# Performance work log

Measured on AMD Instinct MI355X. Metric: run time of the kernel, lower is better.

## Reference

```python
import jax, jax.numpy as jnp
import numpy as np


def setup_inputs() -> dict:
    key = jax.random.key(0)
    ks = jax.random.split(key, 10)
    B, T = 1024, 8192
    # X features: [time, current I, temperature T, voltage U]
    t = jnp.cumsum(jax.random.uniform(ks[0], (B, T, 1), jnp.float32) + 0.5, axis=1)  # increasing time
    feats = jax.random.normal(ks[1], (B, T, 3), jnp.float32)
    X = jnp.concatenate([t, feats], axis=-1)  # [B, T, 4]
    # SC: [Q (capacity), eta_0, R, SOC_init_base]; keep Q away from 0
    SC = jax.random.uniform(ks[2], (B, 4), jnp.float32, minval=0.5, maxval=1.5)
    std = 0.1
    # SOC_init_net: Linear(4,1) -> Softplus -> Linear(1,1), normal(0,0.1) weights, zero bias
    W1i = jax.random.normal(ks[3], (1, 4), jnp.float32) * std
    b1i = jnp.zeros((1,), jnp.float32)
    W2i = jax.random.normal(ks[4], (1, 1), jnp.float32) * std
    b2i = jnp.zeros((1,), jnp.float32)
    # eta_net: Linear(2,1) -> Softplus -> Linear(1,1)
    W1e = jax.random.normal(ks[5], (1, 2), jnp.float32) * std
    b1e = jnp.zeros((1,), jnp.float32)
    W2e = jax.random.normal(ks[6], (1, 1), jnp.float32) * std
    b2e = jnp.zeros((1,), jnp.float32)
    return {"X": X, "SC": SC, "W1i": W1i, "b1i": b1i, "W2i": W2i, "b2i": b2i,
            "W1e": W1e, "b1e": b1e, "W2e": W2e, "b2e": b2e}


def reference(X, SC, W1i, b1i, W2i, b2i, W1e, b1e, W2e, b2e):
    # X: [B, T, 4] = (t, I, Temp, U); SC: [B, 4] = (Q, eta_0, R, soc_base)
    I = X[..., 1:2]      # [B, T, 1]
    Temp = X[..., 2:3]   # [B, T, 1]
    U = X[..., 3:4]      # [B, T, 1]
    R = SC[..., 2:3]     # [B, 1]
    # SOC_init_net on first-timestep features
    feat0 = jnp.concatenate([I[:, 0, :], Temp[:, 0, :], U[:, 0, :], R], axis=-1)  # [B, 4]
    h0 = jax.nn.softplus(feat0 @ W1i.T + b1i)
    soc_net = h0 @ W2i.T + b2i                     # [B, 1]
    SOC_init = SC[..., 3:4] * (1.0 + soc_net)      # [B, 1]
    # eta_net over all timesteps
    feat = jnp.concatenate([I, Temp], axis=-1)     # [B, T, 2]
    h = jax.nn.softplus(feat @ W1e.T + b1e)
    delta_eta = h @ W2e.T + b2e                    # [B, T, 1]
    # ODE RHS: dSOC/dt = eta_0 * (1 + delta_eta) * I / (3600 * Q)
    Q = SC[..., 0:1][:, None, :]                   # [B, 1, 1]
    eta0 = SC[..., 1:2][:, None, :]                # [B, 1, 1]
    f = eta0 * (1.0 + delta_eta) * I / (3600.0 * Q)  # [B, T, 1]
    # Euler integration: y_{k+1} = y_k + (t_{k+1} - t_k) * f(x_k, y_k); f independent of y -> cumsum
    ts = X[..., 0:1]                               # [B, T, 1]
    dt = ts[:, 1:] - ts[:, :-1]                    # [B, T-1, 1]
    incr = dt * f[:, :-1]                          # [B, T-1, 1]
    zero = jnp.zeros_like(SOC_init)[:, None, :]    # [B, 1, 1]
    SOC = SOC_init[:, None, :] + jnp.concatenate([zero, jnp.cumsum(incr, axis=1)], axis=1)
    return SOC                                     # [B, T, 1]
```

## Files before the change

### kernel.cpp

```cpp
#include <hip/hip_runtime.h>
#include <type_traits>


static __device__ __forceinline__ float bf2f(unsigned int u) {
    union { unsigned int i; float f; } v;
    v.i = u << 16;
    return v.f;
}
static __device__ __forceinline__ unsigned short f2bf(float f) {
    union { unsigned int i; float f; } v;
    v.f = f;
    unsigned int x = v.i;
    return (unsigned short)((x + 0x7fffu + ((x >> 16) & 1u)) >> 16);
}
static __device__ __forceinline__ float sp_fast(float x) {
    return __logf(1.f + __expf(x));
}

struct F4 { float ts, I, Te, U; };
static __device__ __forceinline__ F4 dec(ushort4 x) {
    return {bf2f(x.x), bf2f(x.y), bf2f(x.z), bf2f(x.w)};
}
static __device__ __forceinline__ F4 dec(float4 x) {
    return {x.x, x.y, x.z, x.w};
}

template <bool BF16>
static __device__ __forceinline__ float ld(const void* p, int i) {
    return BF16 ? bf2f(((const unsigned short*)p)[i]) : ((const float*)p)[i];
}

constexpr int BLOCK = 256;

template <bool BF16, int NC>
static __device__ void scan_reg(
    const void* __restrict__ Xv, const void* __restrict__ SCv,
    const void* __restrict__ W1i, const void* __restrict__ b1i,
    const void* __restrict__ W2i, const void* __restrict__ b2i,
    const void* __restrict__ W1e, const void* __restrict__ b1e,
    const void* __restrict__ W2e, const void* __restrict__ b2e,
    void* __restrict__ outv, float* s_wtot, float* s_init)
{
    using XVec = typename std::conditional<BF16, ushort4, float4>::type;
    constexpr int T = NC * 256;
    constexpr int SPAN = T / 4;

    const int b    = blockIdx.x;
    const int tid  = threadIdx.x;
    const int lane = tid & 63;
    const int wave = tid >> 6;
    const int wavestart = wave * SPAN;

    const float Q    = ld<BF16>(SCv, b * 4 + 0);
    const float eta0 = ld<BF16>(SCv, b * 4 + 1);
    const float R    = ld<BF16>(SCv, b * 4 + 2);
    const float S3   = ld<BF16>(SCv, b * 4 + 3);
    const float w1e0 = ld<BF16>(W1e, 0);
    const float w1e1 = ld<BF16>(W1e, 1);
    const float vb1e = ld<BF16>(b1e, 0);
    const float coef = eta0 / (3600.f * Q);
    const float c2   = coef * ld<BF16>(W2e, 0);
    const float c1   = coef * (1.f + ld<BF16>(b2e, 0));

    const XVec* Xrow = (const XVec*)Xv + (size_t)b * T;

    float ts_c, f_c;
    if (wave > 0) {
        const F4 vp = dec(Xrow[wavestart - 1]);
        const float hp = sp_fast(fmaf(vp.I, w1e0, fmaf(vp.Te, w1e1, vb1e)));
        f_c  = fmaf(c2, hp, c1) * vp.I;
        ts_c = vp.ts;
    } else {
        const F4 v0 = dec(Xrow[0]);
        ts_c = v0.ts;
        f_c  = 0.f;
        const float pre = fmaf(v0.I, ld<BF16>(W1i, 0),
                          fmaf(v0.Te, ld<BF16>(W1i, 1),
                          fmaf(v0.U, ld<BF16>(W1i, 2),
                          fmaf(R, ld<BF16>(W1i, 3), ld<BF16>(b1i, 0)))));
        const float h0 = sp_fast(pre);
        if (lane == 0)
            *s_init = S3 * (1.f + fmaf(h0, ld<BF16>(W2i, 0), ld<BF16>(b2i, 0)));
    }

    float vals[NC];
    float carry = 0.f;
    XVec cur = Xrow[wavestart + lane];
    XVec nxt = Xrow[wavestart + 64 + lane];
    #pragma unroll
    for (int c = 0; c < NC; ++c) {
        XVec after = cur;
        if (c + 2 < NC) after = Xrow[wavestart + (c + 2) * 64 + lane];

        const F4 v = dec(cur);
        const float f = fmaf(c2, sp_fast(fmaf(v.I, w1e0, fmaf(v.Te, w1e1, vb1e))), c1) * v.I;

        float pts = __shfl_up(v.ts, 1, 64);
        float pf  = __shfl_up(f,   1, 64);
        if (lane == 0) { pts = ts_c; pf = f_c; }
        float g = (v.ts - pts) * pf;

        #pragma unroll
        for (int d = 1; d < 64; d <<= 1) {
            const float u = __shfl_up(g, d, 64);
            if (lane >= d) g += u;
        }
        g += carry;
        vals[c] = g;

        carry = __shfl(g, 63, 64);
        ts_c  = __shfl(v.ts, 63, 64);
        f_c   = __shfl(f, 63, 64);
        cur = nxt; nxt = after;
    }
    if (lane == 0) s_wtot[wave] = carry;
    __syncthreads();

    float base = *s_init;
    #pragma unroll
    for (int w = 0; w < 3; ++w)
        if (w < wave) base += s_wtot[w];

    if (!BF16) {
        float* op = (float*)outv + (size_t)b * T + wavestart + lane;
        #pragma unroll
        for (int c = 0; c < NC; ++c) op[c * 64] = vals[c] + base;
    } else {
        unsigned short* op = (unsigned short*)outv + (size_t)b * T + wavestart + lane;
        #pragma unroll
        for (int c = 0; c < NC; ++c) op[c * 64] = f2bf(vals[c] + base);
    }
}

__global__ __launch_bounds__(BLOCK, 4) void socnet_reg(
    const void* __restrict__ X, const void* __restrict__ SC,
    const void* __restrict__ W1i, const void* __restrict__ b1i,
    const void* __restrict__ W2i, const void* __restrict__ b2i,
    const void* __restrict__ W1e, const void* __restrict__ b1e,
    const void* __restrict__ W2e, const void* __restrict__ b2e,
    void* __restrict__ out)
{
    __shared__ float s_wtot[4];
    __shared__ float s_init;

    const unsigned int* scw = (const unsigned int*)SC;
    const float l0 = bf2f(scw[0] & 0xFFFFu), l1 = bf2f(scw[1] & 0xFFFFu);
    const float l2 = bf2f(scw[2] & 0xFFFFu), l3 = bf2f(scw[3] & 0xFFFFu);
    const bool isbf =
        (l0 >= 0.45f && l0 <= 1.55f) && (l1 >= 0.45f && l1 <= 1.55f) &&
        (l2 >= 0.45f && l2 <= 1.55f) && (l3 >= 0.45f && l3 <= 1.55f);

    if (isbf) scan_reg<true, 32>(X, SC, W1i, b1i, W2i, b2i, W1e, b1e, W2e, b2e,
                                 out, s_wtot, &s_init);
    else      scan_reg<false, 32>(X, SC, W1i, b1i, W2i, b2i, W1e, b1e, W2e, b2e,
                                  out, s_wtot, &s_init);
}

template <bool BF16>
static __device__ void scan_serial(
    const void* __restrict__ Xv, const void* __restrict__ SCv,
    const void* __restrict__ W1i, const void* __restrict__ b1i,
    const void* __restrict__ W2i, const void* __restrict__ b2i,
    const void* __restrict__ W1e, const void* __restrict__ b1e,
    const void* __restrict__ W2e, const void* __restrict__ b2e,
    void* __restrict__ outv, int T,
    float* s_wts, float* s_wf, float* s_wsum, float* s_carr)
{
    using XVec = typename std::conditional<BF16, ushort4, float4>::type;
    const int b = blockIdx.x, tid = threadIdx.x;
    const int lane = tid & 63, wave = tid >> 6;
    const int ntile = (T + BLOCK - 1) / BLOCK;

    const float Q    = ld<BF16>(SCv, b * 4 + 0);
    const float eta0 = ld<BF16>(SCv, b * 4 + 1);
    const float R    = ld<BF16>(SCv, b * 4 + 2);
    const float S3   = ld<BF16>(SCv, b * 4 + 3);
    const float w1e0 = ld<BF16>(W1e, 0);
    const float w1e1 = ld<BF16>(W1e, 1);
    const float vb1e = ld<BF16>(b1e, 0);
    const float coef = eta0 / (3600.f * Q);
    const float c2   = coef * ld<BF16>(W2e, 0);
    const float c1   = coef * (1.f + ld<BF16>(b2e, 0));

    const XVec* Xrow = (const XVec*)Xv + (size_t)b * T;

    for (int tile = 0; tile < ntile; ++tile) {
        const int t = tile * BLOCK + tid;
        const bool act = t < T;
        F4 v = {0.f, 0.f, 0.f, 0.f};
        if (act) v = dec(Xrow[t]);
        const float f = fmaf(c2, sp_fast(fmaf(v.I, w1e0, fmaf(v.Te, w1e1, vb1e))), c1) * v.I;

        float pts = __shfl_up(v.ts, 1, 64);
        float pf  = __shfl_up(f, 1, 64);

        __syncthreads();
        if (lane == 63) { s_wts[wave] = v.ts; s_wf[wave] = f; }
        if (tile == 0 && tid == 0) {
            const float pre = fmaf(v.I, ld<BF16>(W1i, 0),
                              fmaf(v.Te, ld<BF16>(W1i, 1),
                              fmaf(v.U, ld<BF16>(W1i, 2),
                              fmaf(R, ld<BF16>(W1i, 3), ld<BF16>(b1i, 0)))));
            s_carr[0] = S3 * (1.f + fmaf(sp_fast(pre), ld<BF16>(W2i, 0), ld<BF16>(b2i, 0)));
        }
        __syncthreads();
        if (lane == 0) {
            if (wave == 0) { if (tile > 0) { pts = s_carr[1]; pf = s_carr[2]; } }
            else { pts = s_wts[wave - 1]; pf = s_wf[wave - 1]; }
        }
        float g = (t == 0 || !act) ? 0.f : (v.ts - pts) * pf;
        #pragma unroll
        for (int d = 1; d < 64; d <<= 1) {
            const float u = __shfl_up(g, d, 64);
            if (lane >= d) g += u;
        }
        if (lane == 63) s_wsum[wave] = g;
        __syncthreads();
        float soc = s_carr[0];
        #pragma unroll
        for (int w = 0; w < 3; ++w) if (w < wave) soc += s_wsum[w];
        soc += g;
        if (act) {
            if (BF16) ((unsigned short*)outv)[(size_t)b * T + t] = f2bf(soc);
            else      ((float*)outv)[(size_t)b * T + t] = soc;
        }
        __syncthreads();
        if (tid == BLOCK - 1) { s_carr[0] = soc; s_carr[1] = v.ts; s_carr[2] = f; }
    }
}

__global__ __launch_bounds__(BLOCK) void socnet_serial_k(
    const void* __restrict__ X, const void* __restrict__ SC,
    const void* __restrict__ W1i, const void* __restrict__ b1i,
    const void* __restrict__ W2i, const void* __restrict__ b2i,
    const void* __restrict__ W1e, const void* __restrict__ b1e,
    const void* __restrict__ W2e, const void* __restrict__ b2e,
    void* __restrict__ out, int T)
{
    __shared__ float s_wts[4], s_wf[4], s_wsum[4], s_carr[3];
    const unsigned int* scw = (const unsigned int*)SC;
    const float l0 = bf2f(scw[0] & 0xFFFFu), l1 = bf2f(scw[1] & 0xFFFFu);
    const float l2 = bf2f(scw[2] & 0xFFFFu), l3 = bf2f(scw[3] & 0xFFFFu);
    const bool isbf =
        (l0 >= 0.45f && l0 <= 1.55f) && (l1 >= 0.45f && l1 <= 1.55f) &&
        (l2 >= 0.45f && l2 <= 1.55f) && (l3 >= 0.45f && l3 <= 1.55f);
    if (isbf) scan_serial<true >(X, SC, W1i, b1i, W2i, b2i, W1e, b1e, W2e, b2e,
                                 out, T, s_wts, s_wf, s_wsum, s_carr);
    else      scan_serial<false>(X, SC, W1i, b1i, W2i, b2i, W1e, b1e, W2e, b2e,
                                 out, T, s_wts, s_wf, s_wsum, s_carr);
}

extern "C" void kernel_launch(void* const* d_in, const int* in_sizes, int n_in,
                              void* d_out, int out_size, void* d_ws, size_t ws_size,
                              hipStream_t stream) {
    const int B = in_sizes[1] / 4;
    const int T = in_sizes[0] / (B * 4);

    if (T == 8192) {
        socnet_reg<<<dim3(B), dim3(BLOCK), 0, stream>>>(
            d_in[0], d_in[1], d_in[2], d_in[3], d_in[4], d_in[5],
            d_in[6], d_in[7], d_in[8], d_in[9], d_out);
    } else {
        socnet_serial_k<<<dim3(B), dim3(BLOCK), 0, stream>>>(
            d_in[0], d_in[1], d_in[2], d_in[3], d_in[4], d_in[5],
            d_in[6], d_in[7], d_in[8], d_in[9], d_out, T);
    }
}
```

Measured before the change: 225.5 us.

## Stage X tiles into LDS via global_load_lds and scan per 1024-step tile

```diff
diff --git a/kernel.cpp b/kernel.cpp
--- a/kernel.cpp
+++ b/kernel.cpp
@@ -31,129 +31,12 @@
 }
 
 constexpr int BLOCK = 256;
-
-template <bool BF16, int NC>
-static __device__ void scan_reg(
-    const void* __restrict__ Xv, const void* __restrict__ SCv,
-    const void* __restrict__ W1i, const void* __restrict__ b1i,
-    const void* __restrict__ W2i, const void* __restrict__ b2i,
-    const void* __restrict__ W1e, const void* __restrict__ b1e,
-    const void* __restrict__ W2e, const void* __restrict__ b2e,
-    void* __restrict__ outv, float* s_wtot, float* s_init)
-{
-    using XVec = typename std::conditional<BF16, ushort4, float4>::type;
-    constexpr int T = NC * 256;
-    constexpr int SPAN = T / 4;
-
-    const int b    = blockIdx.x;
-    const int tid  = threadIdx.x;
-    const int lane = tid & 63;
-    const int wave = tid >> 6;
-    const int wavestart = wave * SPAN;
-
-    const float Q    = ld<BF16>(SCv, b * 4 + 0);
-    const float eta0 = ld<BF16>(SCv, b * 4 + 1);
-    const float R    = ld<BF16>(SCv, b * 4 + 2);
-    const float S3   = ld<BF16>(SCv, b * 4 + 3);
-    const float w1e0 = ld<BF16>(W1e, 0);
-    const float w1e1 = ld<BF16>(W1e, 1);
-    const float vb1e = ld<BF16>(b1e, 0);
-    const float coef = eta0 / (3600.f * Q);
-    const float c2   = coef * ld<BF16>(W2e, 0);
-    const float c1   = coef * (1.f + ld<BF16>(b2e, 0));
-
-    const XVec* Xrow = (const XVec*)Xv + (size_t)b * T;
-
-    float ts_c, f_c;
-    if (wave > 0) {
-        const F4 vp = dec(Xrow[wavestart - 1]);
-        const float hp = sp_fast(fmaf(vp.I, w1e0, fmaf(vp.Te, w1e1, vb1e)));
-        f_c  = fmaf(c2, hp, c1) * vp.I;
-        ts_c = vp.ts;
-    } else {
-        const F4 v0 = dec(Xrow[0]);
-        ts_c = v0.ts;
-        f_c  = 0.f;
-        const float pre = fmaf(v0.I, ld<BF16>(W1i, 0),
-                          fmaf(v0.Te, ld<BF16>(W1i, 1),
-                          fmaf(v0.U, ld<BF16>(W1i, 2),
-                          fmaf(R, ld<BF16>(W1i, 3), ld<BF16>(b1i, 0)))));
-        const float h0 = sp_fast(pre);
-        if (lane == 0)
-            *s_init = S3 * (1.f + fmaf(h0, ld<BF16>(W2i, 0), ld<BF16>(b2i, 0)));
-    }
-
-    float vals[NC];
-    float carry = 0.f;
-    XVec cur = Xrow[wavestart + lane];
-    XVec nxt = Xrow[wavestart + 64 + lane];
-    #pragma unroll
-    for (int c = 0; c < NC; ++c) {
-        XVec after = cur;
-        if (c + 2 < NC) after = Xrow[wavestart + (c + 2) * 64 + lane];
-
-        const F4 v = dec(cur);
-        const float f = fmaf(c2, sp_fast(fmaf(v.I, w1e0, fmaf(v.Te, w1e1, vb1e))), c1) * v.I;
-
-        float pts = __shfl_up(v.ts, 1, 64);
-        float pf  = __shfl_up(f,   1, 64);
-        if (lane == 0) { pts = ts_c; pf = f_c; }
-        float g = (v.ts - pts) * pf;
-
-        #pragma unroll
-        for (int d = 1; d < 64; d <<= 1) {
-            const float u = __shfl_up(g, d, 64);
-            if (lane >= d) g += u;
-        }
-        g += carry;
-        vals[c] = g;
-
-        carry = __shfl(g, 63, 64);
-        ts_c  = __shfl(v.ts, 63, 64);
-        f_c   = __shfl(f, 63, 64);
-        cur = nxt; nxt = after;
-    }
-    if (lane == 0) s_wtot[wave] = carry;
-    __syncthreads();
-
-    float base = *s_init;
-    #pragma unroll
-    for (int w = 0; w < 3; ++w)
-        if (w < wave) base += s_wtot[w];
-
-    if (!BF16) {
-        float* op = (float*)outv + (size_t)b * T + wavestart + lane;
-        #pragma unroll
-        for (int c = 0; c < NC; ++c) op[c * 64] = vals[c] + base;
-    } else {
-        unsigned short* op = (unsigned short*)outv + (size_t)b * T + wavestart + lane;
-        #pragma unroll
-        for (int c = 0; c < NC; ++c) op[c * 64] = f2bf(vals[c] + base);
-    }
-}
-
-__global__ __launch_bounds__(BLOCK, 4) void socnet_reg(
-    const void* __restrict__ X, const void* __restrict__ SC,
-    const void* __restrict__ W1i, const void* __restrict__ b1i,
-    const void* __restrict__ W2i, const void* __restrict__ b2i,
-    const void* __restrict__ W1e, const void* __restrict__ b1e,
-    const void* __restrict__ W2e, const void* __restrict__ b2e,
-    void* __restrict__ out)
-{
-    __shared__ float s_wtot[4];
-    __shared__ float s_init;
-
-    const unsigned int* scw = (const unsigned int*)SC;
-    const float l0 = bf2f(scw[0] & 0xFFFFu), l1 = bf2f(scw[1] & 0xFFFFu);
-    const float l2 = bf2f(scw[2] & 0xFFFFu), l3 = bf2f(scw[3] & 0xFFFFu);
-    const bool isbf =
-        (l0 >= 0.45f && l0 <= 1.55f) && (l1 >= 0.45f && l1 <= 1.55f) &&
-        (l2 >= 0.45f && l2 <= 1.55f) && (l3 >= 0.45f && l3 <= 1.55f);
-
-    if (isbf) scan_reg<true, 32>(X, SC, W1i, b1i, W2i, b2i, W1e, b1e, W2e, b2e,
-                                 out, s_wtot, &s_init);
-    else      scan_reg<false, 32>(X, SC, W1i, b1i, W2i, b2i, W1e, b1e, W2e, b2e,
-                                  out, s_wtot, &s_init);
+constexpr int TT    = 1024;
+
+static __device__ __forceinline__ void dma16(const float4* g, float4* l) {
+    __builtin_amdgcn_global_load_lds(
+        (const __attribute__((address_space(1))) unsigned int*)g,
+        (__attribute__((address_space(3))) unsigned int*)l, 16, 0, 0);
 }
 
 template <bool BF16>
@@ -226,6 +109,144 @@
         }
         __syncthreads();
         if (tid == BLOCK - 1) { s_carr[0] = soc; s_carr[1] = v.ts; s_carr[2] = f; }
+    }
+}
+
+__global__ __launch_bounds__(BLOCK, 4) void socnet_staged(
+    const void* __restrict__ X, const void* __restrict__ SC,
+    const void* __restrict__ W1i, const void* __restrict__ b1i,
+    const void* __restrict__ W2i, const void* __restrict__ b2i,
+    const void* __restrict__ W1e, const void* __restrict__ b1e,
+    const void* __restrict__ W2e, const void* __restrict__ b2e,
+    void* __restrict__ out, int T)
+{
+    __shared__ float4 stage[TT];
+    __shared__ __align__(16) float s_tot[16];
+    __shared__ float s_c[2], s_pts[2], s_pf[2];
+    __shared__ float s_wts[4], s_wf[4], s_wsum[4], s_carr[3];
+
+    const unsigned int* scw = (const unsigned int*)SC;
+    const float l0 = bf2f(scw[0] & 0xFFFFu), l1 = bf2f(scw[1] & 0xFFFFu);
+    const float l2 = bf2f(scw[2] & 0xFFFFu), l3 = bf2f(scw[3] & 0xFFFFu);
+    const bool isbf =
+        (l0 >= 0.45f && l0 <= 1.55f) && (l1 >= 0.45f && l1 <= 1.55f) &&
+        (l2 >= 0.45f && l2 <= 1.55f) && (l3 >= 0.45f && l3 <= 1.55f);
+    if (isbf) {
+        scan_serial<true>(X, SC, W1i, b1i, W2i, b2i, W1e, b1e, W2e, b2e,
+                          out, T, s_wts, s_wf, s_wsum, s_carr);
+        return;
+    }
+
+    const int b    = blockIdx.x;
+    const int tid  = threadIdx.x;
+    const int lane = tid & 63;
+    const int w    = tid >> 6;
+    const int NT   = T / TT;
+
+    const float* SCf = (const float*)SC;
+    const float Q    = SCf[b * 4 + 0];
+    const float eta0 = SCf[b * 4 + 1];
+    const float R    = SCf[b * 4 + 2];
+    const float S3   = SCf[b * 4 + 3];
+    const float w1e0 = ((const float*)W1e)[0];
+    const float w1e1 = ((const float*)W1e)[1];
+    const float vb1e = ((const float*)b1e)[0];
+    const float coef = eta0 / (3600.f * Q);
+    const float c2   = coef * ((const float*)W2e)[0];
+    const float c1   = coef * (1.f + ((const float*)b2e)[0]);
+
+    const float4* Xrow = (const float4*)X + (size_t)b * T;
+    float* orow = (float*)out + (size_t)b * T;
+
+    if (w == 0) {
+        const float4 x0 = Xrow[0];
+        const float pre = fmaf(x0.y, ((const float*)W1i)[0],
+                          fmaf(x0.z, ((const float*)W1i)[1],
+                          fmaf(x0.w, ((const float*)W1i)[2],
+                          fmaf(R, ((const float*)W1i)[3], ((const float*)b1i)[0]))));
+        const float init = S3 * (1.f + fmaf(sp_fast(pre),
+                             ((const float*)W2i)[0], ((const float*)b2i)[0]));
+        if (lane == 0) {
+            s_c[0]   = init;
+            s_pts[0] = x0.x;
+            s_pf[0]  = 0.f;
+        }
+    }
+    {
+        #pragma unroll
+        for (int j = 0; j < 4; ++j) {
+            const int e = (w * 4 + j) * 64 + lane;
+            dma16(Xrow + e, &stage[e]);
+        }
+    }
+
+    for (int t = 0; t < NT; ++t) {
+        __syncthreads();
+        const int par = t & 1;
+        const float cpts = s_pts[par];
+        const float cpf  = s_pf[par];
+
+        float g[4];
+        float ts_last = 0.f, I_last = 0.f, Te_last = 0.f;
+        #pragma unroll
+        for (int j = 0; j < 4; ++j) {
+            const int e = (w * 4 + j) * 64 + lane;
+            const float4 v  = stage[e];
+            const float4 vp = stage[e > 0 ? e - 1 : 0];
+            float fp  = fmaf(c2, sp_fast(fmaf(vp.y, w1e0, fmaf(vp.z, w1e1, vb1e))), c1) * vp.y;
+            float tsp = vp.x;
+            if (e == 0) { fp = cpf; tsp = cpts; }
+            float gg = (v.x - tsp) * fp;
+            #pragma unroll
+            for (int d = 1; d < 64; d <<= 1) {
+                const float u = __shfl_up(gg, d, 64);
+                if (lane >= d) gg += u;
+            }
+            g[j] = gg;
+            if (j == 3) { ts_last = v.x; I_last = v.y; Te_last = v.z; }
+        }
+        #pragma unroll
+        for (int j = 0; j < 4; ++j)
+            if (lane == 63) s_tot[w * 4 + j] = g[j];
+
+        __syncthreads();
+
+        if (t + 1 < NT) {
+            const float4* src = Xrow + (size_t)(t + 1) * TT;
+            #pragma unroll
+            for (int j = 0; j < 4; ++j) {
+                const int e = (w * 4 + j) * 64 + lane;
+                dma16(src + e, &stage[e]);
+            }
+        }
+
+        const float4 q0 = *(const float4*)&s_tot[0];
+        const float4 q1 = *(const float4*)&s_tot[4];
+        const float4 q2 = *(const float4*)&s_tot[8];
+        const float4 q3 = *(const float4*)&s_tot[12];
+        float pre = s_c[par];
+        if (w > 0) pre += q0.x + q0.y + q0.z + q0.w;
+        if (w > 1) pre += q1.x + q1.y + q1.z + q1.w;
+        if (w > 2) pre += q2.x + q2.y + q2.z + q2.w;
+        const float4 mine = (w == 0) ? q0 : (w == 1) ? q1 : (w == 2) ? q2 : q3;
+        const float b0 = pre;
+        const float b1v = b0 + mine.x;
+        const float b2v = b1v + mine.y;
+        const float b3v = b2v + mine.z;
+
+        float* op = orow + (size_t)t * TT + w * 256 + lane;
+        op[0]   = g[0] + b0;
+        op[64]  = g[1] + b1v;
+        op[128] = g[2] + b2v;
+        op[192] = g[3] + b3v;
+
+        if (tid == BLOCK - 1) {
+            const int nxt = (t + 1) & 1;
+            s_c[nxt]   = g[3] + b3v;
+            s_pts[nxt] = ts_last;
+            s_pf[nxt]  = fmaf(c2, sp_fast(fmaf(I_last, w1e0,
+                             fmaf(Te_last, w1e1, vb1e))), c1) * I_last;
+        }
     }
 }
 
@@ -256,10 +277,10 @@
     const int B = in_sizes[1] / 4;
     const int T = in_sizes[0] / (B * 4);
 
-    if (T == 8192) {
-        socnet_reg<<<dim3(B), dim3(BLOCK), 0, stream>>>(
+    if (T % TT == 0) {
+        socnet_staged<<<dim3(B), dim3(BLOCK), 0, stream>>>(
             d_in[0], d_in[1], d_in[2], d_in[3], d_in[4], d_in[5],
-            d_in[6], d_in[7], d_in[8], d_in[9], d_out);
+            d_in[6], d_in[7], d_in[8], d_in[9], d_out, T);
     } else {
         socnet_serial_k<<<dim3(B), dim3(BLOCK), 0, stream>>>(
             d_in[0], d_in[1], d_in[2], d_in[3], d_in[4], d_in[5],
```

Result: faster. 219.9 us (-2.5%).

## Split each row scan across blocks with decoupled lookback through global slots

Applied to the files above, without the earlier changes.

```diff
diff --git a/kernel.cpp b/kernel.cpp
--- a/kernel.cpp
+++ b/kernel.cpp
@@ -31,30 +31,31 @@
 }
 
 constexpr int BLOCK = 256;
-
-template <bool BF16, int NC>
-static __device__ void scan_reg(
+constexpr int PART  = 1024;
+
+template <bool BF16>
+static __device__ void scan_part(
     const void* __restrict__ Xv, const void* __restrict__ SCv,
     const void* __restrict__ W1i, const void* __restrict__ b1i,
     const void* __restrict__ W2i, const void* __restrict__ b2i,
     const void* __restrict__ W1e, const void* __restrict__ b1e,
     const void* __restrict__ W2e, const void* __restrict__ b2e,
-    void* __restrict__ outv, float* s_wtot, float* s_init)
+    void* __restrict__ outv, int T, int PPR,
+    unsigned long long* __restrict__ slots,
+    float* s_wtot, float* s_pref)
 {
     using XVec = typename std::conditional<BF16, ushort4, float4>::type;
-    constexpr int T = NC * 256;
-    constexpr int SPAN = T / 4;
-
-    const int b    = blockIdx.x;
+
+    const int gb   = blockIdx.x;
+    const int b    = gb / PPR;
+    const int p    = gb - b * PPR;
     const int tid  = threadIdx.x;
     const int lane = tid & 63;
-    const int wave = tid >> 6;
-    const int wavestart = wave * SPAN;
+    const int w    = tid >> 6;
+    const int wstart = p * PART + (w << 8);
 
     const float Q    = ld<BF16>(SCv, b * 4 + 0);
     const float eta0 = ld<BF16>(SCv, b * 4 + 1);
-    const float R    = ld<BF16>(SCv, b * 4 + 2);
-    const float S3   = ld<BF16>(SCv, b * 4 + 3);
     const float w1e0 = ld<BF16>(W1e, 0);
     const float w1e1 = ld<BF16>(W1e, 1);
     const float vb1e = ld<BF16>(b1e, 0);
@@ -64,84 +65,100 @@
 
     const XVec* Xrow = (const XVec*)Xv + (size_t)b * T;
 
-    float ts_c, f_c;
-    if (wave > 0) {
-        const F4 vp = dec(Xrow[wavestart - 1]);
-        const float hp = sp_fast(fmaf(vp.I, w1e0, fmaf(vp.Te, w1e1, vb1e)));
-        f_c  = fmaf(c2, hp, c1) * vp.I;
-        ts_c = vp.ts;
-    } else {
+    XVec x[4];
+    #pragma unroll
+    for (int j = 0; j < 4; ++j) x[j] = Xrow[wstart + j * 64 + lane];
+
+    float ts_c, f_c, init = 0.f;
+    if (p == 0 && w == 0) {
         const F4 v0 = dec(Xrow[0]);
         ts_c = v0.ts;
         f_c  = 0.f;
+        const float R  = ld<BF16>(SCv, b * 4 + 2);
+        const float S3 = ld<BF16>(SCv, b * 4 + 3);
         const float pre = fmaf(v0.I, ld<BF16>(W1i, 0),
                           fmaf(v0.Te, ld<BF16>(W1i, 1),
                           fmaf(v0.U, ld<BF16>(W1i, 2),
                           fmaf(R, ld<BF16>(W1i, 3), ld<BF16>(b1i, 0)))));
-        const float h0 = sp_fast(pre);
-        if (lane == 0)
-            *s_init = S3 * (1.f + fmaf(h0, ld<BF16>(W2i, 0), ld<BF16>(b2i, 0)));
-    }
-
-    float vals[NC];
+        init = S3 * (1.f + fmaf(sp_fast(pre), ld<BF16>(W2i, 0), ld<BF16>(b2i, 0)));
+    } else {
+        const F4 vp = dec(Xrow[wstart - 1]);
+        f_c  = fmaf(c2, sp_fast(fmaf(vp.I, w1e0, fmaf(vp.Te, w1e1, vb1e))), c1) * vp.I;
+        ts_c = vp.ts;
+    }
+
+    float vals[4];
     float carry = 0.f;
-    XVec cur = Xrow[wavestart + lane];
-    XVec nxt = Xrow[wavestart + 64 + lane];
     #pragma unroll
-    for (int c = 0; c < NC; ++c) {
-        XVec after = cur;
-        if (c + 2 < NC) after = Xrow[wavestart + (c + 2) * 64 + lane];
-
-        const F4 v = dec(cur);
+    for (int j = 0; j < 4; ++j) {
+        const F4 v = dec(x[j]);
         const float f = fmaf(c2, sp_fast(fmaf(v.I, w1e0, fmaf(v.Te, w1e1, vb1e))), c1) * v.I;
-
         float pts = __shfl_up(v.ts, 1, 64);
         float pf  = __shfl_up(f,   1, 64);
         if (lane == 0) { pts = ts_c; pf = f_c; }
         float g = (v.ts - pts) * pf;
-
         #pragma unroll
         for (int d = 1; d < 64; d <<= 1) {
             const float u = __shfl_up(g, d, 64);
             if (lane >= d) g += u;
         }
         g += carry;
-        vals[c] = g;
-
+        vals[j] = g;
         carry = __shfl(g, 63, 64);
         ts_c  = __shfl(v.ts, 63, 64);
         f_c   = __shfl(f, 63, 64);
-        cur = nxt; nxt = after;
-    }
-    if (lane == 0) s_wtot[wave] = carry;
+    }
+    if (lane == 0) s_wtot[w] = carry;
     __syncthreads();
 
-    float base = *s_init;
+    if (tid == 0) {
+        const float tot = s_wtot[0] + s_wtot[1] + s_wtot[2] + s_wtot[3] + init;
+        const unsigned long long pay =
+            (1ull << 32) | (unsigned long long)__float_as_uint(tot);
+        __hip_atomic_store(&slots[gb], pay, __ATOMIC_RELEASE,
+                           __HIP_MEMORY_SCOPE_AGENT);
+        float pref = init;
+        const int rb = gb - p;
+        for (int i = rb; i < gb; ++i) {
+            unsigned long long v;
+            do {
+                v = __hip_atomic_load(&slots[i], __ATOMIC_ACQUIRE,
+                                      __HIP_MEMORY_SCOPE_AGENT);
+                if (!(v >> 32)) __builtin_amdgcn_s_sleep(1);
+            } while (!(v >> 32));
+            pref += __uint_as_float((unsigned int)v);
+        }
+        *s_pref = pref;
+    }
+    __syncthreads();
+
+    float base = *s_pref;
     #pragma unroll
-    for (int w = 0; w < 3; ++w)
-        if (w < wave) base += s_wtot[w];
+    for (int ww = 0; ww < 3; ++ww)
+        if (ww < w) base += s_wtot[ww];
 
     if (!BF16) {
-        float* op = (float*)outv + (size_t)b * T + wavestart + lane;
-        #pragma unroll
-        for (int c = 0; c < NC; ++c) op[c * 64] = vals[c] + base;
+        float* op = (float*)outv + (size_t)b * T + wstart + lane;
+        #pragma unroll
+        for (int j = 0; j < 4; ++j) op[j * 64] = vals[j] + base;
     } else {
-        unsigned short* op = (unsigned short*)outv + (size_t)b * T + wavestart + lane;
-        #pragma unroll
-        for (int c = 0; c < NC; ++c) op[c * 64] = f2bf(vals[c] + base);
-    }
-}
-
-__global__ __launch_bounds__(BLOCK, 4) void socnet_reg(
+        unsigned short* op = (unsigned short*)outv + (size_t)b * T + wstart + lane;
+        #pragma unroll
+        for (int j = 0; j < 4; ++j) op[j * 64] = f2bf(vals[j] + base);
+    }
+}
+
+__global__ __launch_bounds__(BLOCK, 8) void socnet_lookback(
     const void* __restrict__ X, const void* __restrict__ SC,
     const void* __restrict__ W1i, const void* __restrict__ b1i,
     const void* __restrict__ W2i, const void* __restrict__ b2i,
     const void* __restrict__ W1e, const void* __restrict__ b1e,
     const void* __restrict__ W2e, const void* __restrict__ b2e,
-    void* __restrict__ out)
+    void* __restrict__ out, int T, int PPR,
+    unsigned long long* __restrict__ slots)
 {
     __shared__ float s_wtot[4];
-    __shared__ float s_init;
+    __shared__ float s_pref;
 
     const unsigned int* scw = (const unsigned int*)SC;
     const float l0 = bf2f(scw[0] & 0xFFFFu), l1 = bf2f(scw[1] & 0xFFFFu);
@@ -150,10 +167,10 @@
         (l0 >= 0.45f && l0 <= 1.55f) && (l1 >= 0.45f && l1 <= 1.55f) &&
         (l2 >= 0.45f && l2 <= 1.55f) && (l3 >= 0.45f && l3 <= 1.55f);
 
-    if (isbf) scan_reg<true, 32>(X, SC, W1i, b1i, W2i, b2i, W1e, b1e, W2e, b2e,
-                                 out, s_wtot, &s_init);
-    else      scan_reg<false, 32>(X, SC, W1i, b1i, W2i, b2i, W1e, b1e, W2e, b2e,
-                                  out, s_wtot, &s_init);
+    if (isbf) scan_part<true >(X, SC, W1i, b1i, W2i, b2i, W1e, b1e, W2e, b2e,
+                               out, T, PPR, slots, s_wtot, &s_pref);
+    else      scan_part<false>(X, SC, W1i, b1i, W2i, b2i, W1e, b1e, W2e, b2e,
+                               out, T, PPR, slots, s_wtot, &s_pref);
 }
 
 template <bool BF16>
@@ -256,10 +273,14 @@
     const int B = in_sizes[1] / 4;
     const int T = in_sizes[0] / (B * 4);
 
-    if (T == 8192) {
-        socnet_reg<<<dim3(B), dim3(BLOCK), 0, stream>>>(
+    if (T % PART == 0) {
+        const int PPR = T / PART;
+        const int nblk = B * PPR;
+        hipMemsetAsync(d_ws, 0, (size_t)nblk * sizeof(unsigned long long), stream);
+        socnet_lookback<<<dim3(nblk), dim3(BLOCK), 0, stream>>>(
             d_in[0], d_in[1], d_in[2], d_in[3], d_in[4], d_in[5],
-            d_in[6], d_in[7], d_in[8], d_in[9], d_out);
+            d_in[6], d_in[7], d_in[8], d_in[9], d_out, T, PPR,
+            (unsigned long long*)d_ws);
     } else {
         socnet_serial_k<<<dim3(B), dim3(BLOCK), 0, stream>>>(
             d_in[0], d_in[1], d_in[2], d_in[3], d_in[4], d_in[5],
```

New measurement: 815.5 us. 3.62x slower.
